# Kernel optimization log

Hardware: AMD Instinct MI355X
Metric: run time of the kernel (lower is better)

The kernel has to match this reference:

```python
import jax, jax.numpy as jnp
import numpy as np


def _conv1x1(x, w, b):
    # x: [B,C,H,W], w: [O,C], b: [O] -> [B,O,H,W]
    return jnp.einsum('bchw,oc->bohw', x, w) + b[None, :, None, None]


def setup_inputs() -> dict:
    key = jax.random.key(0)
    ks = jax.random.split(key, 11)
    B, C, Ci, H, W = 4, 256, 128, 64, 64
    s_in = 1.0 / np.sqrt(C)
    s_ci = 1.0 / np.sqrt(Ci)
    return {
        'x': jax.random.normal(ks[0], (B, C, H, W), jnp.float32),
        'g_w': jax.random.normal(ks[1], (Ci, C), jnp.float32) * s_in,
        'g_b': jax.random.normal(ks[2], (Ci,), jnp.float32) * 0.01,
        'theta_w': jax.random.normal(ks[3], (Ci, C), jnp.float32) * s_in,
        'theta_b': jax.random.normal(ks[4], (Ci,), jnp.float32) * 0.01,
        'phi_w': jax.random.normal(ks[5], (Ci, C), jnp.float32) * s_in,
        'phi_b': jax.random.normal(ks[6], (Ci,), jnp.float32) * 0.01,
        'wz_w': jax.random.normal(ks[7], (C, Ci), jnp.float32) * s_ci,
        'wz_b': jax.random.normal(ks[8], (C,), jnp.float32) * 0.01,
        'bn_gamma': jax.random.uniform(ks[9], (C,), jnp.float32, 0.5, 1.5),
        'bn_beta': jax.random.normal(ks[10], (C,), jnp.float32) * 0.01,
    }


def reference(x, g_w, g_b, theta_w, theta_b, phi_w, phi_b, wz_w, wz_b, bn_gamma, bn_beta):
    B, C, H, W = x.shape
    Ci = g_w.shape[0]
    N = H * W
    # 1x1 conv projections, flattened over spatial positions
    g_x = _conv1x1(x, g_w, g_b).reshape(B, Ci, N).transpose(0, 2, 1)       # [B,N,Ci]
    theta_x = _conv1x1(x, theta_w, theta_b).reshape(B, Ci, N)              # [B,Ci,N]
    phi_x = _conv1x1(x, phi_w, phi_b).reshape(B, Ci, N)                    # [B,Ci,N]
    # f[b, i, j] = theta_i . phi_j  -> [B,N,N]
    f = jnp.einsum('bci,bcj->bij', theta_x, phi_x)
    # NOTE: softmax over dim=1 (query axis) — faithful to original (non-standard)
    f_div_C = jax.nn.softmax(f, axis=1)
    y = jnp.einsum('bij,bjc->bic', f_div_C, g_x)                           # [B,N,Ci]
    y = y.transpose(0, 2, 1).reshape(B, Ci, H, W)                          # [B,Ci,H,W]
    # W_z: 1x1 conv + BatchNorm2d (training-mode batch statistics)
    w_y = _conv1x1(y, wz_w, wz_b)                                          # [B,C,H,W]
    mean = jnp.mean(w_y, axis=(0, 2, 3), keepdims=True)
    var = jnp.var(w_y, axis=(0, 2, 3), keepdims=True)
    w_y = (w_y - mean) * jax.lax.rsqrt(var + 1e-5)
    w_y = w_y * bn_gamma[None, :, None, None] + bn_beta[None, :, None, None]
    return w_y + x
```

## Files before the change

### kernel.cpp

```cpp
#include <hip/hip_runtime.h>


#define B_  4
#define C_  256
#define CI  128
#define N_  4096
#define NB  (B_*N_)
#define ISPLIT 16
#define MB_ (1u<<20)

typedef _Float16 f16;
typedef f16   f16x8 __attribute__((ext_vector_type(8)));
typedef f16   f16x4 __attribute__((ext_vector_type(4)));
typedef float f32x4 __attribute__((ext_vector_type(4)));
typedef float f32x16 __attribute__((ext_vector_type(16)));
typedef unsigned u32x2 __attribute__((ext_vector_type(2)));
typedef unsigned u32x4v __attribute__((ext_vector_type(4)));

#define MFMA(a,b,c)   __builtin_amdgcn_mfma_f32_16x16x32_f16(a,b,c,0,0,0)
#define MFMA32(a,b,c) __builtin_amdgcn_mfma_f32_32x32x16_f16(a,b,c,0,0,0)

#define GLD16(g, lp) __builtin_amdgcn_global_load_lds( \
    (const __attribute__((address_space(1))) void*)(g), \
    (__attribute__((address_space(3))) void*)(lp), 16, 0, 0)

#define OFF_THETA  0
#define OFF_PHI    (4u*MB_)
#define OFF_G      (8u*MB_)
#define OFF_YP     (12u*MB_)
#define OFF_WY     0
#define OFF_MD     (28u*MB_)
#define OFF_PS     (OFF_MD + 65536)
#define OFF_PSUM   (OFF_PS + ISPLIT*NB*4)
#define OFF_SSUM   (OFF_PSUM + 524288)
#define OFF_SSQ    (OFF_SSUM + 1024)
#define OFF_WCVT   (OFF_SSQ + 1024)
#define PSZ ((size_t)B_*N_*CI)

__global__ void k_init(const float* gw, const float* tw, const float* pw,
                       const float* zw, f16* wcvt) {
    int i = blockIdx.x * 256 + threadIdx.x;
    const float* s;
    int which = i >> 15;
    if (which == 0) s = gw; else if (which == 1) s = tw;
    else if (which == 2) s = pw; else s = zw;
    wcvt[i] = (f16)s[i & 32767];
}

__global__ __launch_bounds__(256) void k_proj(
        const float* __restrict__ x, const f16* __restrict__ wcvt,
        const float* __restrict__ gb, const float* __restrict__ tb,
        const float* __restrict__ pb,
        f16* __restrict__ thetaT, f16* __restrict__ phiT, f16* __restrict__ gC) {
    __shared__ __align__(16) f16 xT[32 * 264];
    int bb = blockIdx.x >> 7;
    int n0 = (blockIdx.x & 127) * 32;
    int t = threadIdx.x;

    const float* xb = x + (size_t)bb * C_ * N_;
    for (int rep = 0; rep < 8; rep++) {
        int lin = rep * 256 + t;
        int c = lin >> 3, np = (lin & 7) * 4;
        float4 v = *reinterpret_cast<const float4*>(xb + c * N_ + n0 + np);
        xT[(np + 0) * 264 + c] = (f16)v.x;
        xT[(np + 1) * 264 + c] = (f16)v.y;
        xT[(np + 2) * 264 + c] = (f16)v.z;
        xT[(np + 3) * 264 + c] = (f16)v.w;
    }
    __syncthreads();

    int w = t >> 6, l16 = t & 15, q = (t & 63) >> 4;
    int ci0 = w * 32;
    for (int proj = 0; proj < 3; proj++) {
        const f16* W0 = wcvt + proj * 32768;
        f32x4 acc[2][2] = {};
        for (int kk = 0; kk < 8; kk++) {
            f16x8 a0 = *reinterpret_cast<const f16x8*>(W0 + (ci0 + l16) * 256 + kk * 32 + q * 8);
            f16x8 a1 = *reinterpret_cast<const f16x8*>(W0 + (ci0 + 16 + l16) * 256 + kk * 32 + q * 8);
#pragma unroll
            for (int nt = 0; nt < 2; nt++) {
                f16x8 bv = *reinterpret_cast<const f16x8*>(&xT[(nt * 16 + l16) * 264 + kk * 32 + q * 8]);
                acc[0][nt] = MFMA(a0, bv, acc[0][nt]);
                acc[1][nt] = MFMA(a1, bv, acc[1][nt]);
            }
        }
        const float* bias = (proj == 0) ? gb : (proj == 1) ? tb : pb;
#pragma unroll
        for (int a = 0; a < 2; a++) {
#pragma unroll
            for (int nt = 0; nt < 2; nt++) {
                int n = n0 + nt * 16 + l16;
                int cib = ci0 + a * 16 + q * 4;
                if (proj == 0) {
#pragma unroll
                    for (int r = 0; r < 4; r++)
                        gC[((size_t)bb * CI + cib + r) * N_ + n] = (f16)(acc[a][nt][r] + bias[cib + r]);
                } else {
                    f16x4 v4;
#pragma unroll
                    for (int r = 0; r < 4; r++) v4[r] = (f16)(acc[a][nt][r] + bias[cib + r]);
                    f16* dst = (proj == 1 ? thetaT : phiT) + ((size_t)bb * N_ + n) * CI + cib;
                    *reinterpret_cast<f16x4*>(dst) = v4;
                }
            }
        }
    }
}

__global__ __launch_bounds__(256, 2) void k_cols(
        const f16* __restrict__ thetaT, const f16* __restrict__ phiT,
        float* __restrict__ ps) {
    __shared__ __align__(16) f16 thS[2][64 * 128];
    int id = blockIdx.x;
    int isp = id & 15, jb = (id >> 4) & 15, bb = id >> 8;
    int t = threadIdx.x, w = t >> 6, l = t & 63, l16 = t & 15, q = (t & 63) >> 4;
    int jw0 = jb * 256 + w * 64;

    f16x8 pf[4][4];
    const f16* pb = phiT + ((size_t)bb * N_ + jw0) * CI;
#pragma unroll
    for (int jt = 0; jt < 4; jt++)
#pragma unroll
        for (int kk = 0; kk < 4; kk++)
            pf[jt][kk] = *reinterpret_cast<const f16x8*>(pb + (jt * 16 + l16) * CI + kk * 32 + q * 8);

    const f16* thB = thetaT + ((size_t)bb * N_ + isp * 256) * CI;
    auto stage = [&](int bf, int it0) {
#pragma unroll
        for (int r = 0; r < 4; r++) {
            int p = r * 256 + w * 64 + l;
            int pi = p >> 4, pu = (p & 15) ^ (pi & 15);
            const char* ga = (const char*)(thB + (size_t)(it0 + pi) * CI) + pu * 16;
            GLD16(ga, &thS[bf][(r * 256 + w * 64) * 8]);
        }
    };

    float s[4] = {0.f, 0.f, 0.f, 0.f};
    stage(0, 0);
    __syncthreads();
    for (int it = 0; it < 4; it++) {
        int bf = it & 1;
        if (it + 1 < 4) stage(bf ^ 1, (it + 1) * 64);
#pragma unroll
        for (int ic = 0; ic < 4; ic++) {
            f16x8 av[4];
#pragma unroll
            for (int kk = 0; kk < 4; kk++)
                av[kk] = *reinterpret_cast<const f16x8*>(
                    &thS[bf][(ic * 16 + l16) * 128 + (((kk * 4 + q) ^ l16) * 8)]);
            f32x4 f[4] = {};
#pragma unroll
            for (int kk = 0; kk < 4; kk++)
#pragma unroll
                for (int jt = 0; jt < 4; jt++)
                    f[jt] = MFMA(av[kk], pf[jt][kk], f[jt]);
#pragma unroll
            for (int jt = 0; jt < 4; jt++)
                s[jt] += __expf(f[jt][0]) + __expf(f[jt][1])
                       + __expf(f[jt][2]) + __expf(f[jt][3]);
        }
        __syncthreads();
    }
#pragma unroll
    for (int jt = 0; jt < 4; jt++) {
        s[jt] += __shfl_xor(s[jt], 16);
        s[jt] += __shfl_xor(s[jt], 32);
    }
    if (q == 0) {
#pragma unroll
        for (int jt = 0; jt < 4; jt++)
            ps[isp * NB + bb * N_ + jw0 + jt * 16 + l16] = s[jt];
    }
}

__global__ void k_colmerge(const float* __restrict__ ps, float* __restrict__ md) {
    int j = blockIdx.x * 256 + threadIdx.x;
    float s = 0.f;
    for (int isp = 0; isp < ISPLIT; isp++) s += ps[isp * NB + j];
    md[j] = __logf(s);
}

__global__ __launch_bounds__(256, 2) void k_attn(
        const f16* __restrict__ thetaT, const f16* __restrict__ phiT,
        const f16* __restrict__ gC, const float* __restrict__ md,
        f16* __restrict__ yP) {
    __shared__ __align__(16) char smem[65536];
    f16 (*phiS)[64 * 128] = (f16(*)[64 * 128])smem;
    f16 (*gS)[128 * 64]   = (f16(*)[128 * 64])(smem + 32768);
    f16* yTr = (f16*)smem;

    int jq = blockIdx.x & 3;
    int ib = blockIdx.x >> 2;
    int bb = ib >> 5;
    int i0 = (ib & 31) * 128;
    int t = threadIdx.x, w = t >> 6, l = t & 63;
    int l31 = l & 31, hi = l >> 5;
    int jbase = jq * 1024;

    f16x8 ta[8];
    const f16* tb = thetaT + ((size_t)bb * N_ + i0 + w * 32 + l31) * CI + hi * 8;
#pragma unroll
    for (int kk = 0; kk < 8; kk++)
        ta[kk] = *reinterpret_cast<const f16x8*>(tb + kk * 16);

    const f16* phiB = phiT + (size_t)bb * N_ * CI;
    const f16* gB   = gC   + (size_t)bb * CI * N_;
    const float* mdb = md + bb * N_;

    auto stage = [&](int bf, int j0g) {
#pragma unroll
        for (int r = 0; r < 4; r++) {
            int p = r * 256 + w * 64 + l;
            int ub = (r * 256 + w * 64) * 8;
            int pj = p >> 4, pu = (p & 15) ^ (pj & 15);
            const char* ga = (const char*)(phiB + (size_t)(j0g + pj) * CI) + pu * 16;
            GLD16(ga, &phiS[bf][ub]);
            int pc = p >> 3, pu2 = (p & 7) ^ (pc & 7);
            const char* ga2 = (const char*)(gB + (size_t)pc * N_ + j0g) + pu2 * 16;
            GLD16(ga2, &gS[bf][ub]);
        }
    };

    f32x16 yacc[4] = {};
    stage(0, jbase);
    __syncthreads();
    for (int jt = 0; jt < 16; jt++) {
        int bf = jt & 1;
        if (jt + 1 < 16) stage(bf ^ 1, jbase + (jt + 1) * 64);

        float mdv[2][16];
#pragma unroll
        for (int js = 0; js < 2; js++)
#pragma unroll
            for (int c = 0; c < 4; c++) {
                float4 v = *reinterpret_cast<const float4*>(
                    mdb + jbase + jt * 64 + js * 32 + c * 8 + hi * 4);
                mdv[js][c * 4 + 0] = v.x; mdv[js][c * 4 + 1] = v.y;
                mdv[js][c * 4 + 2] = v.z; mdv[js][c * 4 + 3] = v.w;
            }

        f32x16 facc[2] = {};
#pragma unroll
        for (int kk = 0; kk < 8; kk++) {
#pragma unroll
            for (int js = 0; js < 2; js++) {
                f16x8 pv = *reinterpret_cast<const f16x8*>(
                    &phiS[bf][(js * 32 + l31) * 128 + (((kk * 2 + hi) ^ (l31 & 15)) * 8)]);
                facc[js] = MFMA32(pv, ta[kk], facc[js]);
            }
        }

#pragma unroll
        for (int js = 0; js < 2; js++) {
#pragma unroll
            for (int ch = 0; ch < 2; ch++) {
                float e0 = __expf(facc[js][ch * 8 + 0] - mdv[js][ch * 8 + 0]);
                float e1 = __expf(facc[js][ch * 8 + 1] - mdv[js][ch * 8 + 1]);
                float e2 = __expf(facc[js][ch * 8 + 2] - mdv[js][ch * 8 + 2]);
                float e3 = __expf(facc[js][ch * 8 + 3] - mdv[js][ch * 8 + 3]);
                float e4 = __expf(facc[js][ch * 8 + 4] - mdv[js][ch * 8 + 4]);
                float e5 = __expf(facc[js][ch * 8 + 5] - mdv[js][ch * 8 + 5]);
                float e6 = __expf(facc[js][ch * 8 + 6] - mdv[js][ch * 8 + 6]);
                float e7 = __expf(facc[js][ch * 8 + 7] - mdv[js][ch * 8 + 7]);
                unsigned p01 = __builtin_bit_cast(unsigned, __builtin_amdgcn_cvt_pkrtz(e0, e1));
                unsigned p23 = __builtin_bit_cast(unsigned, __builtin_amdgcn_cvt_pkrtz(e2, e3));
                unsigned p45 = __builtin_bit_cast(unsigned, __builtin_amdgcn_cvt_pkrtz(e4, e5));
                unsigned p67 = __builtin_bit_cast(unsigned, __builtin_amdgcn_cvt_pkrtz(e6, e7));
                u32x2 s0 = __builtin_amdgcn_permlane32_swap(p01, p45, false, false);
                u32x2 s1 = __builtin_amdgcn_permlane32_swap(p23, p67, false, false);
                u32x4v wu = {s0[0], s1[0], s0[1], s1[1]};
                f16x8 wfr = __builtin_bit_cast(f16x8, wu);
                int jc = js * 2 + ch;
#pragma unroll
                for (int cs = 0; cs < 4; cs++) {
                    f16x8 gv = *reinterpret_cast<const f16x8*>(
                        &gS[bf][(cs * 32 + l31) * 64 + (((jc * 2 + hi) ^ (l31 & 7)) * 8)]);
                    yacc[cs] = MFMA32(wfr, gv, yacc[cs]);
                }
            }
        }
        __syncthreads();
    }

    f16* yw = yTr + w * (32 * 136);
#pragma unroll
    for (int cs = 0; cs < 4; cs++)
#pragma unroll
        for (int r = 0; r < 16; r++)
            yw[((r & 3) + 8 * (r >> 2) + 4 * hi) * 136 + cs * 32 + l31] = (f16)yacc[cs][r];
    f16* yo = yP + (size_t)jq * PSZ + ((size_t)bb * N_ + i0 + w * 32) * CI;
#pragma unroll
    for (int rr = 0; rr < 8; rr++) {
        int chunk = rr * 64 + l;
        int il = chunk >> 4, u = chunk & 15;
        *reinterpret_cast<f16x8*>(yo + il * CI + u * 8) =
            *reinterpret_cast<const f16x8*>(&yw[il * 136 + u * 8]);
    }
}

__global__ __launch_bounds__(256) void k_wz(
        const f16* __restrict__ wzc, const f16* __restrict__ yP,
        const float* __restrict__ zb, f16* __restrict__ wy,
        float* __restrict__ psum) {
    int id = blockIdx.x;
    int nb = id & 63, bb = id >> 6;
    int t = threadIdx.x, w = t >> 6, l16 = t & 15, q = (t & 63) >> 4;
    int o0 = w * 64, n0 = nb * 64;
    f32x4 acc[4][4] = {};
#pragma unroll
    for (int kk = 0; kk < 4; kk++) {
        f16x8 bv[4];
#pragma unroll
        for (int nt = 0; nt < 4; nt++) {
            size_t yi = ((size_t)bb * N_ + n0 + nt * 16 + l16) * CI + kk * 32 + q * 8;
            f16x8 b0 = *reinterpret_cast<const f16x8*>(yP + yi);
            f16x8 b1 = *reinterpret_cast<const f16x8*>(yP + PSZ + yi);
            f16x8 b2 = *reinterpret_cast<const f16x8*>(yP + 2 * PSZ + yi);
            f16x8 b3 = *reinterpret_cast<const f16x8*>(yP + 3 * PSZ + yi);
            bv[nt] = (b0 + b1) + (b2 + b3);
        }
#pragma unroll
        for (int os = 0; os < 4; os++) {
            f16x8 av = *reinterpret_cast<const f16x8*>(
                wzc + (o0 + os * 16 + l16) * CI + kk * 32 + q * 8);
#pragma unroll
            for (int nt = 0; nt < 4; nt++)
                acc[os][nt] = MFMA(av, bv[nt], acc[os][nt]);
        }
    }
#pragma unroll
    for (int os = 0; os < 4; os++)
#pragma unroll
    for (int r = 0; r < 4; r++) {
        int o = o0 + os * 16 + q * 4 + r;
        float bias = zb[o];
        float sr = 0.f, qr = 0.f;
#pragma unroll
        for (int nt = 0; nt < 4; nt++) {
            float v = acc[os][nt][r] + bias;
            wy[((size_t)bb * C_ + o) * N_ + n0 + nt * 16 + l16] = (f16)v;
            sr += v; qr += v * v;
        }
#pragma unroll
        for (int off = 1; off < 16; off <<= 1) {
            sr += __shfl_xor(sr, off);
            qr += __shfl_xor(qr, off);
        }
        if (l16 == 0) {
            psum[(o * 2 + 0) * 256 + id] = sr;
            psum[(o * 2 + 1) * 256 + id] = qr;
        }
    }
}

__global__ void k_red(const float* __restrict__ psum, float* __restrict__ ssum,
                      float* __restrict__ ssq) {
    int b = blockIdx.x;
    int o = threadIdx.x;
    const float* src = psum + (o * 2 + b) * 256;
    float s = 0.f;
    for (int k = 0; k < 64; k++) {
        float4 v = reinterpret_cast<const float4*>(src)[k];
        s += v.x + v.y + v.z + v.w;
    }
    (b == 0 ? ssum : ssq)[o] = s;
}

__global__ void k_final(const f16* __restrict__ wy, const float* __restrict__ x,
                        const float* __restrict__ ssum, const float* __restrict__ ssq,
                        const float* __restrict__ gamma, const float* __restrict__ beta,
                        float* __restrict__ out) {
    int p = blockIdx.x * 256 + threadIdx.x;
    int c = (p >> 9) & 255;
    const float inv = 1.0f / 16384.0f;
    float mean = ssum[c] * inv;
    float var = ssq[c] * inv - mean * mean;
    float s = gamma[c] * rsqrtf(var + 1e-5f);
    float h = beta[c] - mean * s;
    f16x8 wv = reinterpret_cast<const f16x8*>(wy)[p];
    float4 x0 = reinterpret_cast<const float4*>(x)[2 * p];
    float4 x1 = reinterpret_cast<const float4*>(x)[2 * p + 1];
    float4 o0, o1;
    o0.x = (float)wv[0] * s + h + x0.x;
    o0.y = (float)wv[1] * s + h + x0.y;
    o0.z = (float)wv[2] * s + h + x0.z;
    o0.w = (float)wv[3] * s + h + x0.w;
    o1.x = (float)wv[4] * s + h + x1.x;
    o1.y = (float)wv[5] * s + h + x1.y;
    o1.z = (float)wv[6] * s + h + x1.z;
    o1.w = (float)wv[7] * s + h + x1.w;
    reinterpret_cast<float4*>(out)[2 * p] = o0;
    reinterpret_cast<float4*>(out)[2 * p + 1] = o1;
}

extern "C" void kernel_launch(void* const* d_in, const int* in_sizes, int n_in,
                              void* d_out, int out_size, void* d_ws, size_t ws_size,
                              hipStream_t stream) {
    const float* x     = (const float*)d_in[0];
    const float* gw    = (const float*)d_in[1];
    const float* gb    = (const float*)d_in[2];
    const float* tw    = (const float*)d_in[3];
    const float* tbv   = (const float*)d_in[4];
    const float* pw    = (const float*)d_in[5];
    const float* pb    = (const float*)d_in[6];
    const float* zw    = (const float*)d_in[7];
    const float* zb    = (const float*)d_in[8];
    const float* gamma = (const float*)d_in[9];
    const float* beta  = (const float*)d_in[10];

    char* ws = (char*)d_ws;
    f16* thetaT = (f16*)(ws + OFF_THETA);
    f16* phiT   = (f16*)(ws + OFF_PHI);
    f16* gC     = (f16*)(ws + OFF_G);
    f16* yP     = (f16*)(ws + OFF_YP);
    f16* wy     = (f16*)(ws + OFF_WY);
    f16* wcvt   = (f16*)(ws + OFF_WCVT);
    float* md   = (float*)(ws + OFF_MD);
    float* ps   = (float*)(ws + OFF_PS);
    float* psum = (float*)(ws + OFF_PSUM);
    float* ssum = (float*)(ws + OFF_SSUM);
    float* ssq  = (float*)(ws + OFF_SSQ);

    k_init<<<512, 256, 0, stream>>>(gw, tw, pw, zw, wcvt);
    k_proj<<<512, 256, 0, stream>>>(x, wcvt, gb, tbv, pb, thetaT, phiT, gC);
    k_cols<<<1024, 256, 0, stream>>>(thetaT, phiT, ps);
    k_colmerge<<<64, 256, 0, stream>>>(ps, md);
    k_attn<<<512, 256, 0, stream>>>(thetaT, phiT, gC, md, yP);
    k_wz<<<256, 256, 0, stream>>>(wcvt + 3 * 32768, yP, zb, wy, psum);
    k_red<<<2, 256, 0, stream>>>(psum, ssum, ssq);
    k_final<<<2048, 256, 0, stream>>>(wy, x, ssum, ssq, gamma, beta, (float*)d_out);
}
```

Before: 202.8 us.

## Fold log2e into theta, use exp2 and preload bias into MFMA accumulators

Theta is prescaled by log2(e) in the projection, so both softmax passes can use the native exp2 instruction. The column normalizer is stored as a negative log2, and k_attn seeds the MFMA accumulator with it, which removes the per-element subtraction. k_cols is rebuilt around 32x32 MFMAs with half-width column blocks, twice the grid and a higher occupancy target, and s_setprio hints are wrapped around the MFMA sections. The risks are changed f16 rounding of the scaled theta and extra register pressure at four blocks per CU.

```diff
diff --git a/kernel.cpp b/kernel.cpp
--- a/kernel.cpp
+++ b/kernel.cpp
@@ -8,6 +8,7 @@
 #define NB  (B_*N_)
 #define ISPLIT 16
 #define MB_ (1u<<20)
+#define LOG2E 1.442695041f
 
 typedef _Float16 f16;
 typedef f16   f16x8 __attribute__((ext_vector_type(8)));
@@ -85,6 +86,7 @@
             }
         }
         const float* bias = (proj == 0) ? gb : (proj == 1) ? tb : pb;
+        float scl = (proj == 1) ? LOG2E : 1.0f;
 #pragma unroll
         for (int a = 0; a < 2; a++) {
 #pragma unroll
@@ -98,7 +100,8 @@
                 } else {
                     f16x4 v4;
 #pragma unroll
-                    for (int r = 0; r < 4; r++) v4[r] = (f16)(acc[a][nt][r] + bias[cib + r]);
+                    for (int r = 0; r < 4; r++)
+                        v4[r] = (f16)((acc[a][nt][r] + bias[cib + r]) * scl);
                     f16* dst = (proj == 1 ? thetaT : phiT) + ((size_t)bb * N_ + n) * CI + cib;
                     *reinterpret_cast<f16x4*>(dst) = v4;
                 }
@@ -107,22 +110,21 @@
     }
 }
 
-__global__ __launch_bounds__(256, 2) void k_cols(
+__global__ __launch_bounds__(256, 4) void k_cols(
         const f16* __restrict__ thetaT, const f16* __restrict__ phiT,
         float* __restrict__ ps) {
     __shared__ __align__(16) f16 thS[2][64 * 128];
     int id = blockIdx.x;
-    int isp = id & 15, jb = (id >> 4) & 15, bb = id >> 8;
-    int t = threadIdx.x, w = t >> 6, l = t & 63, l16 = t & 15, q = (t & 63) >> 4;
-    int jw0 = jb * 256 + w * 64;
-
-    f16x8 pf[4][4];
-    const f16* pb = phiT + ((size_t)bb * N_ + jw0) * CI;
-#pragma unroll
-    for (int jt = 0; jt < 4; jt++)
-#pragma unroll
-        for (int kk = 0; kk < 4; kk++)
-            pf[jt][kk] = *reinterpret_cast<const f16x8*>(pb + (jt * 16 + l16) * CI + kk * 32 + q * 8);
+    int isp = id & 15, jb = (id >> 4) & 31, bb = id >> 9;
+    int t = threadIdx.x, w = t >> 6, l = t & 63;
+    int l31 = l & 31, hi = l >> 5;
+    int jw = jb * 128 + w * 32 + l31;
+
+    f16x8 pf[8];
+    const f16* pb = phiT + ((size_t)bb * N_ + jw) * CI + hi * 8;
+#pragma unroll
+    for (int kk = 0; kk < 8; kk++)
+        pf[kk] = *reinterpret_cast<const f16x8*>(pb + kk * 16);
 
     const f16* thB = thetaT + ((size_t)bb * N_ + isp * 256) * CI;
     auto stage = [&](int bf, int it0) {
@@ -135,49 +137,41 @@
         }
     };
 
-    float s[4] = {0.f, 0.f, 0.f, 0.f};
+    float s = 0.f;
     stage(0, 0);
     __syncthreads();
     for (int it = 0; it < 4; it++) {
         int bf = it & 1;
         if (it + 1 < 4) stage(bf ^ 1, (it + 1) * 64);
 #pragma unroll
-        for (int ic = 0; ic < 4; ic++) {
-            f16x8 av[4];
-#pragma unroll
-            for (int kk = 0; kk < 4; kk++)
+        for (int it2 = 0; it2 < 2; it2++) {
+            f16x8 av[8];
+#pragma unroll
+            for (int kk = 0; kk < 8; kk++)
                 av[kk] = *reinterpret_cast<const f16x8*>(
-                    &thS[bf][(ic * 16 + l16) * 128 + (((kk * 4 + q) ^ l16) * 8)]);
-            f32x4 f[4] = {};
-#pragma unroll
-            for (int kk = 0; kk < 4; kk++)
-#pragma unroll
-                for (int jt = 0; jt < 4; jt++)
-                    f[jt] = MFMA(av[kk], pf[jt][kk], f[jt]);
-#pragma unroll
-            for (int jt = 0; jt < 4; jt++)
-                s[jt] += __expf(f[jt][0]) + __expf(f[jt][1])
-                       + __expf(f[jt][2]) + __expf(f[jt][3]);
+                    &thS[bf][(it2 * 32 + l31) * 128 + (((kk * 2 + hi) ^ (l31 & 15)) * 8)]);
+            f32x16 f = {};
+            __builtin_amdgcn_s_setprio(1);
+#pragma unroll
+            for (int kk = 0; kk < 8; kk++)
+                f = MFMA32(av[kk], pf[kk], f);
+            __builtin_amdgcn_s_setprio(0);
+#pragma unroll
+            for (int r = 0; r < 16; r++)
+                s += __builtin_amdgcn_exp2f(f[r]);
         }
         __syncthreads();
     }
-#pragma unroll
-    for (int jt = 0; jt < 4; jt++) {
-        s[jt] += __shfl_xor(s[jt], 16);
-        s[jt] += __shfl_xor(s[jt], 32);
-    }
-    if (q == 0) {
-#pragma unroll
-        for (int jt = 0; jt < 4; jt++)
-            ps[isp * NB + bb * N_ + jw0 + jt * 16 + l16] = s[jt];
-    }
+    s += __shfl_xor(s, 32);
+    if (hi == 0)
+        ps[isp * NB + bb * N_ + jw] = s;
 }
 
 __global__ void k_colmerge(const float* __restrict__ ps, float* __restrict__ md) {
     int j = blockIdx.x * 256 + threadIdx.x;
     float s = 0.f;
     for (int isp = 0; isp < ISPLIT; isp++) s += ps[isp * NB + j];
-    md[j] = __logf(s);
+    md[j] = -__log2f(s);
 }
 
 __global__ __launch_bounds__(256, 2) void k_attn(
@@ -228,18 +222,18 @@
         int bf = jt & 1;
         if (jt + 1 < 16) stage(bf ^ 1, jbase + (jt + 1) * 64);
 
-        float mdv[2][16];
+        f32x16 facc[2];
 #pragma unroll
         for (int js = 0; js < 2; js++)
 #pragma unroll
             for (int c = 0; c < 4; c++) {
                 float4 v = *reinterpret_cast<const float4*>(
                     mdb + jbase + jt * 64 + js * 32 + c * 8 + hi * 4);
-                mdv[js][c * 4 + 0] = v.x; mdv[js][c * 4 + 1] = v.y;
-                mdv[js][c * 4 + 2] = v.z; mdv[js][c * 4 + 3] = v.w;
+                facc[js][c * 4 + 0] = v.x; facc[js][c * 4 + 1] = v.y;
+                facc[js][c * 4 + 2] = v.z; facc[js][c * 4 + 3] = v.w;
             }
 
-        f32x16 facc[2] = {};
+        __builtin_amdgcn_s_setprio(1);
 #pragma unroll
         for (int kk = 0; kk < 8; kk++) {
 #pragma unroll
@@ -249,19 +243,20 @@
                 facc[js] = MFMA32(pv, ta[kk], facc[js]);
             }
         }
+        __builtin_amdgcn_s_setprio(0);
 
 #pragma unroll
         for (int js = 0; js < 2; js++) {
 #pragma unroll
             for (int ch = 0; ch < 2; ch++) {
-                float e0 = __expf(facc[js][ch * 8 + 0] - mdv[js][ch * 8 + 0]);
-                float e1 = __expf(facc[js][ch * 8 + 1] - mdv[js][ch * 8 + 1]);
-                float e2 = __expf(facc[js][ch * 8 + 2] - mdv[js][ch * 8 + 2]);
-                float e3 = __expf(facc[js][ch * 8 + 3] - mdv[js][ch * 8 + 3]);
-                float e4 = __expf(facc[js][ch * 8 + 4] - mdv[js][ch * 8 + 4]);
-                float e5 = __expf(facc[js][ch * 8 + 5] - mdv[js][ch * 8 + 5]);
-                float e6 = __expf(facc[js][ch * 8 + 6] - mdv[js][ch * 8 + 6]);
-                float e7 = __expf(facc[js][ch * 8 + 7] - mdv[js][ch * 8 + 7]);
+                float e0 = __builtin_amdgcn_exp2f(facc[js][ch * 8 + 0]);
+                float e1 = __builtin_amdgcn_exp2f(facc[js][ch * 8 + 1]);
+                float e2 = __builtin_amdgcn_exp2f(facc[js][ch * 8 + 2]);
+                float e3 = __builtin_amdgcn_exp2f(facc[js][ch * 8 + 3]);
+                float e4 = __builtin_amdgcn_exp2f(facc[js][ch * 8 + 4]);
+                float e5 = __builtin_amdgcn_exp2f(facc[js][ch * 8 + 5]);
+                float e6 = __builtin_amdgcn_exp2f(facc[js][ch * 8 + 6]);
+                float e7 = __builtin_amdgcn_exp2f(facc[js][ch * 8 + 7]);
                 unsigned p01 = __builtin_bit_cast(unsigned, __builtin_amdgcn_cvt_pkrtz(e0, e1));
                 unsigned p23 = __builtin_bit_cast(unsigned, __builtin_amdgcn_cvt_pkrtz(e2, e3));
                 unsigned p45 = __builtin_bit_cast(unsigned, __builtin_amdgcn_cvt_pkrtz(e4, e5));
@@ -271,12 +266,14 @@
                 u32x4v wu = {s0[0], s1[0], s0[1], s1[1]};
                 f16x8 wfr = __builtin_bit_cast(f16x8, wu);
                 int jc = js * 2 + ch;
+                __builtin_amdgcn_s_setprio(1);
 #pragma unroll
                 for (int cs = 0; cs < 4; cs++) {
                     f16x8 gv = *reinterpret_cast<const f16x8*>(
                         &gS[bf][(cs * 32 + l31) * 64 + (((jc * 2 + hi) ^ (l31 & 7)) * 8)]);
                     yacc[cs] = MFMA32(wfr, gv, yacc[cs]);
                 }
+                __builtin_amdgcn_s_setprio(0);
             }
         }
         __syncthreads();
@@ -423,7 +420,7 @@
 
     k_init<<<512, 256, 0, stream>>>(gw, tw, pw, zw, wcvt);
     k_proj<<<512, 256, 0, stream>>>(x, wcvt, gb, tbv, pb, thetaT, phiT, gC);
-    k_cols<<<1024, 256, 0, stream>>>(thetaT, phiT, ps);
+    k_cols<<<2048, 256, 0, stream>>>(thetaT, phiT, ps);
     k_colmerge<<<64, 256, 0, stream>>>(ps, md);
     k_attn<<<512, 256, 0, stream>>>(thetaT, phiT, gC, md, yP);
     k_wz<<<256, 256, 0, stream>>>(wcvt + 3 * 32768, yP, zb, wy, psum);
```

Result: no change. 201.0 us (-0.9%).
